# Performance work log

Measured on AMD Instinct MI355X. Metric: run time of the kernel, lower is better.

## Reference

```python
import jax, jax.numpy as jnp
import numpy as np

N_USERS = 50000
DEG = 32
N_EDGES = N_USERS * DEG  # 1,600,000
N_SERVERS = 512


def segment_softmax(x, seg, num_segments):
    # PyG-style scatter softmax over segments defined by seg.
    m = jax.ops.segment_max(x, seg, num_segments=num_segments)
    e = jnp.exp(x - m[seg])
    s = jax.ops.segment_sum(e, seg, num_segments=num_segments) + 1e-16
    return e / s[seg]


def setup_inputs() -> dict:
    key = jax.random.key(0)
    k1, k2, k3, k4, k5, k6, k7 = jax.random.split(key, 7)
    # learned parameters (torch.rand init), shape [E, 1]
    task_allocation = jax.random.uniform(k1, (N_EDGES, 1), dtype=jnp.float32)
    power_allocation = jax.random.uniform(k2, (N_EDGES, 1), dtype=jnp.float32)
    comp_allocation = jax.random.uniform(k3, (N_EDGES, 1), dtype=jnp.float32)
    compute_resource = jax.random.uniform(k4, (N_SERVERS,), dtype=jnp.float32) + 0.5
    path_losses = jax.random.uniform(k5, (N_EDGES,), dtype=jnp.float32) + 0.1
    task_size = jax.random.uniform(k6, (N_USERS,), dtype=jnp.float32) + 0.1
    # user index sorted (each user has DEG edges); server index random
    user_index = jnp.repeat(jnp.arange(N_USERS, dtype=jnp.int64), DEG)
    server_index = jax.random.randint(k7, (N_EDGES,), 0, N_SERVERS, dtype=jnp.int64)
    edge_index = jnp.stack([user_index, server_index], axis=0)
    return {
        "compute_resource": compute_resource,
        "path_losses": path_losses,
        "task_size": task_size,
        "edge_index": edge_index,
        "task_allocation": task_allocation,
        "power_allocation": power_allocation,
        "comp_allocation": comp_allocation,
    }


def reference(compute_resource, path_losses, task_size, edge_index,
              task_allocation, power_allocation, comp_allocation):
    epsilon = 1e-9
    extre = 1e-20
    n_users = task_size.shape[0]
    n_servers = compute_resource.shape[0]
    user_index = edge_index[0]
    server_index = edge_index[1]

    task_sche = segment_softmax(task_allocation[:, 0], user_index, n_users)
    power_sche = segment_softmax(power_allocation[:, 0], user_index, n_users)
    comp_sche = segment_softmax(comp_allocation[:, 0], user_index, n_users)

    tasks = task_size[user_index] * task_sche            # [E]
    comp = compute_resource[server_index] * comp_sche     # [E]
    pw = power_sche * path_losses                         # [E]

    # per-server total received power, broadcast back to edges
    pws = jax.ops.segment_sum(pw, server_index, num_segments=n_servers)[server_index]
    interference = pws - pw
    rate = jnp.log2(1.0 + pw / (interference + epsilon))

    time_loss = tasks / (rate + extre) + tasks / (comp + extre)  # [E]
    per_user = jax.ops.segment_sum(time_loss, user_index, num_segments=n_users)
    return per_user.mean()
```

## Files before the change

kernel.cpp:

```cpp
#include <hip/hip_runtime.h>
#include <math.h>

#define NSRV 512
#define C_CHUNKS 16

__device__ __forceinline__ float quad_sum(float v) {
    int x = __float_as_int(v);
    int y = __builtin_amdgcn_update_dpp(0, x, 0xB1, 0xF, 0xF, true);
    v += __int_as_float(y);
    x = __float_as_int(v);
    y = __builtin_amdgcn_update_dpp(0, x, 0x4E, 0xF, 0xF, true);
    v += __int_as_float(y);
    return v;
}

__device__ __forceinline__ float fast_rcp(float x) {
    return __builtin_amdgcn_rcpf(x);
}

__global__ __launch_bounds__(256) void mmse_pws_part(
    const float* __restrict__ power_alloc,
    const float* __restrict__ path_losses,
    const int*   __restrict__ server_index,
    float*       __restrict__ P,
    int n_edges) {
    __shared__ float bins[NSRV];
    for (int i = threadIdx.x; i < NSRV; i += 256) bins[i] = 0.0f;
    __syncthreads();

    const int t = blockIdx.x * 256 + threadIdx.x;
    if (t * 8 < n_edges) {
        const float4* pa4 = (const float4*)power_alloc;
        const float4* pl4 = (const float4*)path_losses;
        const int4*   si4 = (const int4*)server_index;

        float4 a = pa4[2 * t], b = pa4[2 * t + 1];
        float e0 = __expf(a.x), e1 = __expf(a.y), e2 = __expf(a.z), e3 = __expf(a.w);
        float e4 = __expf(b.x), e5 = __expf(b.y), e6 = __expf(b.z), e7 = __expf(b.w);
        float s = ((e0 + e1) + (e2 + e3)) + ((e4 + e5) + (e6 + e7));
        float inv = fast_rcp(quad_sum(s) + 1e-16f);

        float4 l0 = pl4[2 * t], l1 = pl4[2 * t + 1];
        int4   s0 = si4[2 * t], s1 = si4[2 * t + 1];

        atomicAdd(&bins[s0.x], e0 * inv * l0.x);
        atomicAdd(&bins[s0.y], e1 * inv * l0.y);
        atomicAdd(&bins[s0.z], e2 * inv * l0.z);
        atomicAdd(&bins[s0.w], e3 * inv * l0.w);
        atomicAdd(&bins[s1.x], e4 * inv * l1.x);
        atomicAdd(&bins[s1.y], e5 * inv * l1.y);
        atomicAdd(&bins[s1.z], e6 * inv * l1.z);
        atomicAdd(&bins[s1.w], e7 * inv * l1.w);
    }
    __syncthreads();

    float* dst = P + (size_t)blockIdx.x * NSRV;
    for (int i = threadIdx.x; i < NSRV; i += 256) dst[i] = bins[i];
}

__global__ __launch_bounds__(256) void mmse_reduce(
    const float* __restrict__ P,
    float*       __restrict__ P2,
    float*       __restrict__ out,
    int NB, int chunk) {
    const int g = blockIdx.x * 256 + threadIdx.x;
    if (g == 0) *out = 0.0f;
    const int s = g & (NSRV - 1);
    const int c = g >> 9;
    const int b0 = c * chunk;
    const int b1 = min(b0 + chunk, NB);
    float sum = 0.0f;
#pragma unroll 4
    for (int b = b0; b < b1; ++b) sum += P[(size_t)b * NSRV + s];
    P2[(size_t)c * NSRV + s] = sum;
}

__global__ __launch_bounds__(256) void mmse_loss(
    const float* __restrict__ task_alloc,
    const float* __restrict__ power_alloc,
    const float* __restrict__ comp_alloc,
    const float* __restrict__ path_losses,
    const int*   __restrict__ server_index,
    const float* __restrict__ task_size,
    const float* __restrict__ compute_resource,
    const float* __restrict__ P2,
    float*       __restrict__ out,
    int n_edges, float inv_users) {
    __shared__ float s_cr[NSRV], s_pws[NSRV];
    __shared__ float blocksum;
    for (int i = threadIdx.x; i < NSRV; i += 256) {
        s_cr[i] = compute_resource[i];
        float acc = 0.0f;
#pragma unroll
        for (int c = 0; c < C_CHUNKS; ++c) acc += P2[(size_t)c * NSRV + i];
        s_pws[i] = acc;
    }
    if (threadIdx.x == 0) blocksum = 0.0f;
    __syncthreads();

    const int t = blockIdx.x * 256 + threadIdx.x;
    float tl = 0.0f;
    if (t * 8 < n_edges) {
        const float4* ta4 = (const float4*)task_alloc;
        const float4* pa4 = (const float4*)power_alloc;
        const float4* ca4 = (const float4*)comp_alloc;
        const float4* pl4 = (const float4*)path_losses;
        const int4*   si4 = (const int4*)server_index;

        float4 tA = ta4[2 * t], tB = ta4[2 * t + 1];
        float4 pA = pa4[2 * t], pB = pa4[2 * t + 1];
        float4 cA = ca4[2 * t], cB = ca4[2 * t + 1];
        float4 lA = pl4[2 * t], lB = pl4[2 * t + 1];
        int4   sA = si4[2 * t], sB = si4[2 * t + 1];

        float et[8] = {__expf(tA.x), __expf(tA.y), __expf(tA.z), __expf(tA.w),
                       __expf(tB.x), __expf(tB.y), __expf(tB.z), __expf(tB.w)};
        float ep[8] = {__expf(pA.x), __expf(pA.y), __expf(pA.z), __expf(pA.w),
                       __expf(pB.x), __expf(pB.y), __expf(pB.z), __expf(pB.w)};
        float ec[8] = {__expf(cA.x), __expf(cA.y), __expf(cA.z), __expf(cA.w),
                       __expf(cB.x), __expf(cB.y), __expf(cB.z), __expf(cB.w)};
        float pl[8] = {lA.x, lA.y, lA.z, lA.w, lB.x, lB.y, lB.z, lB.w};
        int   sv[8] = {sA.x, sA.y, sA.z, sA.w, sB.x, sB.y, sB.z, sB.w};

        float st = 0.f, sp = 0.f, sc = 0.f;
#pragma unroll
        for (int k = 0; k < 8; ++k) { st += et[k]; sp += ep[k]; sc += ec[k]; }
        float ist = fast_rcp(quad_sum(st) + 1e-16f);
        float isp = fast_rcp(quad_sum(sp) + 1e-16f);
        float isc = fast_rcp(quad_sum(sc) + 1e-16f);

        const float tsz = task_size[t >> 2];

#pragma unroll
        for (int k = 0; k < 8; ++k) {
            int   srv    = sv[k];
            float tasks  = tsz * (et[k] * ist);
            float comp   = s_cr[srv] * (ec[k] * isc);
            float pw     = (ep[k] * isp) * pl[k];
            float interf = s_pws[srv] - pw;
            float rate   = __log2f(1.0f + pw * fast_rcp(interf + 1e-9f));
            tl += tasks * fast_rcp(rate + 1e-20f) + tasks * fast_rcp(comp + 1e-20f);
        }
    }

    tl = quad_sum(tl);
    if ((threadIdx.x & 3) == 0 && tl != 0.0f) atomicAdd(&blocksum, tl);
    __syncthreads();
    if (threadIdx.x == 0) atomicAdd(out, blocksum * inv_users);
}

extern "C" void kernel_launch(void* const* d_in, const int* in_sizes, int n_in,
                              void* d_out, int out_size, void* d_ws, size_t ws_size,
                              hipStream_t stream) {
    const float* compute_resource = (const float*)d_in[0];
    const float* path_losses      = (const float*)d_in[1];
    const float* task_size        = (const float*)d_in[2];
    const int*   edge_index       = (const int*)d_in[3];
    const float* task_alloc       = (const float*)d_in[4];
    const float* power_alloc      = (const float*)d_in[5];
    const float* comp_alloc       = (const float*)d_in[6];

    const int n_edges = in_sizes[1];
    const int n_users = in_sizes[2];
    const int* server_index = edge_index + n_edges;

    const int groups = n_edges / 8;
    const int NB     = (groups + 255) / 256;
    const int chunk  = (NB + C_CHUNKS - 1) / C_CHUNKS;

    float* P  = (float*)d_ws;
    float* P2 = P + (size_t)NB * NSRV;

    mmse_pws_part<<<NB, 256, 0, stream>>>(
        power_alloc, path_losses, server_index, P, n_edges);

    mmse_reduce<<<(NSRV * C_CHUNKS) / 256, 256, 0, stream>>>(
        P, P2, (float*)d_out, NB, chunk);

    mmse_loss<<<NB, 256, 0, stream>>>(
        task_alloc, power_alloc, comp_alloc, path_losses, server_index,
        task_size, compute_resource, P2, (float*)d_out,
        n_edges, 1.0f / (float)n_users);
}
```

Before: 116.6 us.

## Fuse three kernels into one cooperative kernel with grid-wide syncs

Merges the per-server power partial sums, the chunked reduction and the loss computation into one cooperative kernel separated by two grid syncs. The per-edge received power and server indices stay in registers across phases, so power_alloc, path_losses and server_index are read once instead of twice, and two kernel launches go away. In exchange, all 782 blocks must be co-resident (launch bounds raised to 4 blocks per CU), and the grid-wide barriers add their own synchronisation cost.

```diff
diff --git a/kernel.cpp b/kernel.cpp
--- a/kernel.cpp
+++ b/kernel.cpp
@@ -1,5 +1,8 @@
 #include <hip/hip_runtime.h>
+#include <hip/hip_cooperative_groups.h>
 #include <math.h>
+
+namespace cg = cooperative_groups;
 
 #define NSRV 512
 #define C_CHUNKS 16
@@ -18,18 +21,37 @@
     return __builtin_amdgcn_rcpf(x);
 }
 
-__global__ __launch_bounds__(256) void mmse_pws_part(
+__global__ __launch_bounds__(256, 4) void mmse_fused(
+    const float* __restrict__ task_alloc,
     const float* __restrict__ power_alloc,
+    const float* __restrict__ comp_alloc,
     const float* __restrict__ path_losses,
     const int*   __restrict__ server_index,
+    const float* __restrict__ task_size,
+    const float* __restrict__ compute_resource,
     float*       __restrict__ P,
-    int n_edges) {
-    __shared__ float bins[NSRV];
-    for (int i = threadIdx.x; i < NSRV; i += 256) bins[i] = 0.0f;
+    float*       __restrict__ P2,
+    float*       __restrict__ out,
+    int n_edges, int NB, int chunk, float inv_users) {
+    __shared__ float s_bins[NSRV];
+    __shared__ float s_cr[NSRV];
+    __shared__ float s_blocksum;
+
+    const int tid = threadIdx.x;
+    const int bid = blockIdx.x;
+    for (int i = tid; i < NSRV; i += 256) {
+        s_cr[i]   = compute_resource[i];
+        s_bins[i] = 0.0f;
+    }
+    if (bid == 0 && tid == 0) *out = 0.0f;
     __syncthreads();
 
-    const int t = blockIdx.x * 256 + threadIdx.x;
-    if (t * 8 < n_edges) {
+    const int  t      = bid * 256 + tid;
+    const bool active = (t * 8 < n_edges);
+
+    float pw[8];
+    int   sv[8];
+    if (active) {
         const float4* pa4 = (const float4*)power_alloc;
         const float4* pl4 = (const float4*)path_losses;
         const int4*   si4 = (const int4*)server_index;
@@ -37,96 +59,68 @@
         float4 a = pa4[2 * t], b = pa4[2 * t + 1];
         float e0 = __expf(a.x), e1 = __expf(a.y), e2 = __expf(a.z), e3 = __expf(a.w);
         float e4 = __expf(b.x), e5 = __expf(b.y), e6 = __expf(b.z), e7 = __expf(b.w);
-        float s = ((e0 + e1) + (e2 + e3)) + ((e4 + e5) + (e6 + e7));
+        float s   = ((e0 + e1) + (e2 + e3)) + ((e4 + e5) + (e6 + e7));
         float inv = fast_rcp(quad_sum(s) + 1e-16f);
 
         float4 l0 = pl4[2 * t], l1 = pl4[2 * t + 1];
         int4   s0 = si4[2 * t], s1 = si4[2 * t + 1];
-
-        atomicAdd(&bins[s0.x], e0 * inv * l0.x);
-        atomicAdd(&bins[s0.y], e1 * inv * l0.y);
-        atomicAdd(&bins[s0.z], e2 * inv * l0.z);
-        atomicAdd(&bins[s0.w], e3 * inv * l0.w);
-        atomicAdd(&bins[s1.x], e4 * inv * l1.x);
-        atomicAdd(&bins[s1.y], e5 * inv * l1.y);
-        atomicAdd(&bins[s1.z], e6 * inv * l1.z);
-        atomicAdd(&bins[s1.w], e7 * inv * l1.w);
+        sv[0] = s0.x; sv[1] = s0.y; sv[2] = s0.z; sv[3] = s0.w;
+        sv[4] = s1.x; sv[5] = s1.y; sv[6] = s1.z; sv[7] = s1.w;
+        pw[0] = e0 * inv * l0.x; pw[1] = e1 * inv * l0.y;
+        pw[2] = e2 * inv * l0.z; pw[3] = e3 * inv * l0.w;
+        pw[4] = e4 * inv * l1.x; pw[5] = e5 * inv * l1.y;
+        pw[6] = e6 * inv * l1.z; pw[7] = e7 * inv * l1.w;
+#pragma unroll
+        for (int k = 0; k < 8; ++k) atomicAdd(&s_bins[sv[k]], pw[k]);
     }
     __syncthreads();
+    {
+        float* dst = P + (size_t)bid * NSRV;
+        for (int i = tid; i < NSRV; i += 256) dst[i] = s_bins[i];
+    }
 
-    float* dst = P + (size_t)blockIdx.x * NSRV;
-    for (int i = threadIdx.x; i < NSRV; i += 256) dst[i] = bins[i];
-}
+    cg::this_grid().sync();
 
-__global__ __launch_bounds__(256) void mmse_reduce(
-    const float* __restrict__ P,
-    float*       __restrict__ P2,
-    float*       __restrict__ out,
-    int NB, int chunk) {
-    const int g = blockIdx.x * 256 + threadIdx.x;
-    if (g == 0) *out = 0.0f;
-    const int s = g & (NSRV - 1);
-    const int c = g >> 9;
-    const int b0 = c * chunk;
-    const int b1 = min(b0 + chunk, NB);
-    float sum = 0.0f;
+    if (bid < (C_CHUNKS * NSRV) / 256) {
+        const int g  = bid * 256 + tid;
+        const int s  = g & (NSRV - 1);
+        const int c  = g >> 9;
+        const int b0 = c * chunk;
+        const int b1 = min(b0 + chunk, NB);
+        float sum = 0.0f;
 #pragma unroll 4
-    for (int b = b0; b < b1; ++b) sum += P[(size_t)b * NSRV + s];
-    P2[(size_t)c * NSRV + s] = sum;
-}
+        for (int b = b0; b < b1; ++b) sum += P[(size_t)b * NSRV + s];
+        P2[(size_t)c * NSRV + s] = sum;
+    }
 
-__global__ __launch_bounds__(256) void mmse_loss(
-    const float* __restrict__ task_alloc,
-    const float* __restrict__ power_alloc,
-    const float* __restrict__ comp_alloc,
-    const float* __restrict__ path_losses,
-    const int*   __restrict__ server_index,
-    const float* __restrict__ task_size,
-    const float* __restrict__ compute_resource,
-    const float* __restrict__ P2,
-    float*       __restrict__ out,
-    int n_edges, float inv_users) {
-    __shared__ float s_cr[NSRV], s_pws[NSRV];
-    __shared__ float blocksum;
-    for (int i = threadIdx.x; i < NSRV; i += 256) {
-        s_cr[i] = compute_resource[i];
+    cg::this_grid().sync();
+
+    for (int i = tid; i < NSRV; i += 256) {
         float acc = 0.0f;
 #pragma unroll
         for (int c = 0; c < C_CHUNKS; ++c) acc += P2[(size_t)c * NSRV + i];
-        s_pws[i] = acc;
+        s_bins[i] = acc;
     }
-    if (threadIdx.x == 0) blocksum = 0.0f;
+    if (tid == 0) s_blocksum = 0.0f;
     __syncthreads();
 
-    const int t = blockIdx.x * 256 + threadIdx.x;
     float tl = 0.0f;
-    if (t * 8 < n_edges) {
+    if (active) {
         const float4* ta4 = (const float4*)task_alloc;
-        const float4* pa4 = (const float4*)power_alloc;
         const float4* ca4 = (const float4*)comp_alloc;
-        const float4* pl4 = (const float4*)path_losses;
-        const int4*   si4 = (const int4*)server_index;
 
         float4 tA = ta4[2 * t], tB = ta4[2 * t + 1];
-        float4 pA = pa4[2 * t], pB = pa4[2 * t + 1];
         float4 cA = ca4[2 * t], cB = ca4[2 * t + 1];
-        float4 lA = pl4[2 * t], lB = pl4[2 * t + 1];
-        int4   sA = si4[2 * t], sB = si4[2 * t + 1];
 
         float et[8] = {__expf(tA.x), __expf(tA.y), __expf(tA.z), __expf(tA.w),
                        __expf(tB.x), __expf(tB.y), __expf(tB.z), __expf(tB.w)};
-        float ep[8] = {__expf(pA.x), __expf(pA.y), __expf(pA.z), __expf(pA.w),
-                       __expf(pB.x), __expf(pB.y), __expf(pB.z), __expf(pB.w)};
         float ec[8] = {__expf(cA.x), __expf(cA.y), __expf(cA.z), __expf(cA.w),
                        __expf(cB.x), __expf(cB.y), __expf(cB.z), __expf(cB.w)};
-        float pl[8] = {lA.x, lA.y, lA.z, lA.w, lB.x, lB.y, lB.z, lB.w};
-        int   sv[8] = {sA.x, sA.y, sA.z, sA.w, sB.x, sB.y, sB.z, sB.w};
 
-        float st = 0.f, sp = 0.f, sc = 0.f;
+        float st = 0.f, sc = 0.f;
 #pragma unroll
-        for (int k = 0; k < 8; ++k) { st += et[k]; sp += ep[k]; sc += ec[k]; }
+        for (int k = 0; k < 8; ++k) { st += et[k]; sc += ec[k]; }
         float ist = fast_rcp(quad_sum(st) + 1e-16f);
-        float isp = fast_rcp(quad_sum(sp) + 1e-16f);
         float isc = fast_rcp(quad_sum(sc) + 1e-16f);
 
         const float tsz = task_size[t >> 2];
@@ -136,17 +130,16 @@
             int   srv    = sv[k];
             float tasks  = tsz * (et[k] * ist);
             float comp   = s_cr[srv] * (ec[k] * isc);
-            float pw     = (ep[k] * isp) * pl[k];
-            float interf = s_pws[srv] - pw;
-            float rate   = __log2f(1.0f + pw * fast_rcp(interf + 1e-9f));
+            float interf = s_bins[srv] - pw[k];
+            float rate   = __log2f(1.0f + pw[k] * fast_rcp(interf + 1e-9f));
             tl += tasks * fast_rcp(rate + 1e-20f) + tasks * fast_rcp(comp + 1e-20f);
         }
     }
 
     tl = quad_sum(tl);
-    if ((threadIdx.x & 3) == 0 && tl != 0.0f) atomicAdd(&blocksum, tl);
+    if ((tid & 3) == 0 && tl != 0.0f) atomicAdd(&s_blocksum, tl);
     __syncthreads();
-    if (threadIdx.x == 0) atomicAdd(out, blocksum * inv_users);
+    if (tid == 0) atomicAdd(out, s_blocksum * inv_users);
 }
 
 extern "C" void kernel_launch(void* const* d_in, const int* in_sizes, int n_in,
@@ -168,17 +161,18 @@
     const int NB     = (groups + 255) / 256;
     const int chunk  = (NB + C_CHUNKS - 1) / C_CHUNKS;
 
-    float* P  = (float*)d_ws;
-    float* P2 = P + (size_t)NB * NSRV;
+    float* P   = (float*)d_ws;
+    float* P2  = P + (size_t)NB * NSRV;
+    float* out = (float*)d_out;
+    float  inv_users = 1.0f / (float)n_users;
+    int    ne = n_edges, nb = NB, ck = chunk;
 
-    mmse_pws_part<<<NB, 256, 0, stream>>>(
-        power_alloc, path_losses, server_index, P, n_edges);
-
-    mmse_reduce<<<(NSRV * C_CHUNKS) / 256, 256, 0, stream>>>(
-        P, P2, (float*)d_out, NB, chunk);
-
-    mmse_loss<<<NB, 256, 0, stream>>>(
-        task_alloc, power_alloc, comp_alloc, path_losses, server_index,
-        task_size, compute_resource, P2, (float*)d_out,
-        n_edges, 1.0f / (float)n_users);
+    void* args[] = {
+        (void*)&task_alloc, (void*)&power_alloc, (void*)&comp_alloc,
+        (void*)&path_losses, (void*)&server_index, (void*)&task_size,
+        (void*)&compute_resource, (void*)&P, (void*)&P2, (void*)&out,
+        (void*)&ne, (void*)&nb, (void*)&ck, (void*)&inv_users,
+    };
+    hipLaunchCooperativeKernel((const void*)mmse_fused, dim3(NB), dim3(256),
+                               args, 0, stream);
 }
```

Result: slower. 257.7 us (+121.0%).
